# Kernel optimization log

Hardware: AMD Instinct MI355X
Metric: run time of the kernel (lower is better)

## Reference

```python
import jax, jax.numpy as jnp
import numpy as np

B, N, D_IN, D_OUT = 16, 512, 64, 64
TEMP = 1.0
BN_EPS = 1e-5


def setup_inputs() -> dict:
    key = jax.random.key(0)
    ks = jax.random.split(key, 9)
    s_in = 1.0 / np.sqrt(D_IN)
    return {
        "x": jax.random.normal(ks[0], (B, N, D_IN), dtype=jnp.float32),
        # att_proj: Linear(in_dim, out_dim)
        "W_att_proj": jax.random.uniform(ks[1], (D_OUT, D_IN), jnp.float32, -s_in, s_in),
        "b_att_proj": jax.random.uniform(ks[2], (D_OUT,), jnp.float32, -s_in, s_in),
        # att_weight: xavier_normal_ on (out_dim, 1)
        "att_weight": jax.random.normal(ks[3], (D_OUT, 1), jnp.float32) * np.sqrt(2.0 / (D_OUT + 1)),
        "W_with": jax.random.uniform(ks[4], (D_OUT, D_IN), jnp.float32, -s_in, s_in),
        "b_with": jax.random.uniform(ks[5], (D_OUT,), jnp.float32, -s_in, s_in),
        "W_without": jax.random.uniform(ks[6], (D_OUT, D_IN), jnp.float32, -s_in, s_in),
        "b_without": jax.random.uniform(ks[7], (D_OUT,), jnp.float32, -s_in, s_in),
        # BatchNorm1d affine params
        "gamma": jnp.ones((D_OUT,), jnp.float32),
        "beta": jnp.zeros((D_OUT,), jnp.float32),
    }


def reference(x, W_att_proj, b_att_proj, att_weight, W_with, b_with, W_without, b_without, gamma, beta):
    # dropout is identity (eval). Pairwise elementwise product: (B, N_i, N_j, D_in)
    p = x[:, :, None, :] * x[:, None, :, :]
    # score MLP: linear -> tanh -> linear(out_dim -> 1)
    h = jnp.tanh(jnp.einsum("bijd,od->bijo", p, W_att_proj) + b_att_proj)
    s = jnp.einsum("bijo,o->bij", h, att_weight[:, 0]) / TEMP
    # softmax over j (torch dim=-2 of (B,N,N,1))
    a = jax.nn.softmax(s, axis=2)
    # weighted aggregate + projections
    agg = jnp.einsum("bij,bjd->bid", a, x)
    x_out = agg @ W_with.T + b_with + x @ W_without.T + b_without
    # BatchNorm1d over flattened (B*N, D_out), training-mode batch stats
    flat = x_out.reshape(-1, D_OUT)
    mean = jnp.mean(flat, axis=0)
    var = jnp.var(flat, axis=0)
    normed = (flat - mean) * jax.lax.rsqrt(var + BN_EPS) * gamma + beta
    return jax.nn.selu(normed.reshape(B, N, D_OUT))
```

## Files before the change

### kernel.cpp

```cpp
#include <hip/hip_runtime.h>
#include <hip/hip_bf16.h>

#define BB 16
#define NN 512
#define DD 64
#define BN_ROWS (BB * NN)
#define NBIN 32

typedef unsigned short ushort;
typedef unsigned int uint;
typedef short bf16x8 __attribute__((ext_vector_type(8)));
typedef float f32x4  __attribute__((ext_vector_type(4)));

#define K2LOG2E 2.885390081777927f


__device__ __forceinline__ uint pkbf2(float lo, float hi) {
    union { float f; uint u; } a, b; a.f = lo; b.f = hi;
    return __builtin_amdgcn_perm(b.u + 0x8000u, a.u + 0x8000u, 0x07060302u);
}
__device__ __forceinline__ float bflo(uint u) {
    union { uint i; float f; } c; c.i = u << 16; return c.f;
}
__device__ __forceinline__ float bfhi(uint u) {
    union { uint i; float f; } c; c.i = u & 0xffff0000u; return c.f;
}
__device__ __forceinline__ float sigr(float x) {
    return __builtin_amdgcn_rcpf(__builtin_amdgcn_exp2f(x) + 1.0f);
}

__global__ __launch_bounds__(256) void prep_kernel(
    const float* __restrict__ x, const float* __restrict__ Wp,
    float* __restrict__ wpf, ushort* __restrict__ xbf, float* __restrict__ stats)
{
    const int tid = blockIdx.x * 256 + threadIdx.x;
    const int b = tid >> 12, rem = tid & 4095;
    const int jt = rem >> 7, ks = (rem >> 6) & 1, lane = rem & 63;
    const int qd = lane >> 4, ln = lane & 15;
    const float* __restrict__ src =
        x + ((size_t)(b * NN + jt * 16 + ln)) * DD + ks * 32 + qd * 8;
    const float4 v0 = *(const float4*)src;
    const float4 v1 = *(const float4*)(src + 4);
    uint4 o;
    o.x = pkbf2(v0.x, v0.y); o.y = pkbf2(v0.z, v0.w);
    o.z = pkbf2(v1.x, v1.y); o.w = pkbf2(v1.z, v1.w);
    ((uint4*)xbf)[tid] = o;
    if (tid < DD * DD) {
        const int oo = tid >> 6, d = tid & 63;
        const int mt = oo >> 4, l2 = oo & 15;
        const int k2 = d >> 5, q2 = (d >> 3) & 3, e = d & 7;
        wpf[(((mt * 2 + k2) * 64) + (q2 * 16 + l2)) * 8 + e] = Wp[tid] * K2LOG2E;
    }
    if (tid < NBIN * 128) stats[tid] = 0.0f;
}

template <int MINW>
__global__ __launch_bounds__(256, MINW) void attn_kernel(
    const float* __restrict__ x,  const float* __restrict__ wpf,
    const ushort* __restrict__ xbf,
    const float* __restrict__ bp, const float* __restrict__ aw,
    const float* __restrict__ W1, const float* __restrict__ b1,
    const float* __restrict__ W2, const float* __restrict__ b2,
    float* __restrict__ out, float* __restrict__ stats)
{
    __shared__ float part[4][DD];
    __shared__ float s_esum[4];
    __shared__ __align__(16) float s_agg[DD], s_xi[DD];

    const int t = threadIdx.x;
    const int wv = t >> 6, lane = t & 63;
    const int blk = blockIdx.x;
    const int b = (blk & 7) * 2 + ((blk >> 3) & 1);
    const int i = blk >> 4;
    const int row = b * NN + i;
    const int qd = lane >> 4, ln = lane & 15;
    const ushort* __restrict__ xb16 = xbf + (size_t)b * (NN * DD);
    const float* __restrict__ xrow = x + (size_t)row * DD;

    if (t < DD) s_xi[t] = xrow[t];

    float xiv[2][8];
    #pragma unroll
    for (int ks = 0; ks < 2; ++ks) {
        const float4 a = *(const float4*)(xrow + ks * 32 + qd * 8);
        const float4 c = *(const float4*)(xrow + ks * 32 + qd * 8 + 4);
        xiv[ks][0]=a.x; xiv[ks][1]=a.y; xiv[ks][2]=a.z; xiv[ks][3]=a.w;
        xiv[ks][4]=c.x; xiv[ks][5]=c.y; xiv[ks][6]=c.z; xiv[ks][7]=c.w;
    }

    float bpk[16], awk[16];
    #pragma unroll
    for (int mt = 0; mt < 4; ++mt) {
        const float4 vb = *(const float4*)(bp + mt * 16 + qd * 4);
        const float4 va = *(const float4*)(aw + mt * 16 + qd * 4);
        bpk[mt*4+0] = vb.x * K2LOG2E; bpk[mt*4+1] = vb.y * K2LOG2E;
        bpk[mt*4+2] = vb.z * K2LOG2E; bpk[mt*4+3] = vb.w * K2LOG2E;
        awk[mt*4+0] = va.x * -K2LOG2E; awk[mt*4+1] = va.y * -K2LOG2E;
        awk[mt*4+2] = va.z * -K2LOG2E; awk[mt*4+3] = va.w * -K2LOG2E;
    }

    bf16x8 afrag[8];
    #pragma unroll
    for (int g = 0; g < 8; ++g) {
        const int ks = g & 1;
        const float4 wa = *(const float4*)(wpf + (g * 64 + lane) * 8);
        const float4 wb = *(const float4*)(wpf + (g * 64 + lane) * 8 + 4);
        union { bf16x8 v; uint u[4]; } p;
        p.u[0] = pkbf2(wa.x * xiv[ks][0], wa.y * xiv[ks][1]);
        p.u[1] = pkbf2(wa.z * xiv[ks][2], wa.w * xiv[ks][3]);
        p.u[2] = pkbf2(wb.x * xiv[ks][4], wb.y * xiv[ks][5]);
        p.u[3] = pkbf2(wb.z * xiv[ks][6], wb.w * xiv[ks][7]);
        afrag[g] = p.v;
    }

    float vacc[16];
    #pragma unroll
    for (int k = 0; k < 16; ++k) vacc[k] = 0.0f;
    float esum = 0.0f;

    #pragma unroll 4
    for (int tt = 0; tt < 8; ++tt) {
        const int tile = wv * 8 + tt;
        union { bf16x8 v; uint4 u; } b0, b1u;
        b0.v  = *(const bf16x8*)(xb16 + ((tile * 2 + 0) * 64 + lane) * 8);
        b1u.v = *(const bf16x8*)(xb16 + ((tile * 2 + 1) * 64 + lane) * 8);

        float s0 = 0.0f, s1 = 0.0f, s2 = 0.0f, s3 = 0.0f;
        #pragma unroll
        for (int mt = 0; mt < 4; ++mt) {
            f32x4 acc = { bpk[mt*4+0], bpk[mt*4+1], bpk[mt*4+2], bpk[mt*4+3] };
            acc = __builtin_amdgcn_mfma_f32_16x16x32_bf16(afrag[mt*2+0], b0.v,  acc, 0, 0, 0);
            acc = __builtin_amdgcn_mfma_f32_16x16x32_bf16(afrag[mt*2+1], b1u.v, acc, 0, 0, 0);
            s0 = fmaf(awk[mt*4+0], sigr(acc[0]), s0);
            s1 = fmaf(awk[mt*4+1], sigr(acc[1]), s1);
            s2 = fmaf(awk[mt*4+2], sigr(acc[2]), s2);
            s3 = fmaf(awk[mt*4+3], sigr(acc[3]), s3);
        }
        float sj = (s0 + s1) + (s2 + s3);
        sj += __shfl_xor(sj, 16);
        sj += __shfl_xor(sj, 32);

        const float e = __builtin_amdgcn_exp2f(sj);
        esum += e;
        vacc[0]  = fmaf(e, bflo(b0.u.x),  vacc[0]);
        vacc[1]  = fmaf(e, bfhi(b0.u.x),  vacc[1]);
        vacc[2]  = fmaf(e, bflo(b0.u.y),  vacc[2]);
        vacc[3]  = fmaf(e, bfhi(b0.u.y),  vacc[3]);
        vacc[4]  = fmaf(e, bflo(b0.u.z),  vacc[4]);
        vacc[5]  = fmaf(e, bfhi(b0.u.z),  vacc[5]);
        vacc[6]  = fmaf(e, bflo(b0.u.w),  vacc[6]);
        vacc[7]  = fmaf(e, bfhi(b0.u.w),  vacc[7]);
        vacc[8]  = fmaf(e, bflo(b1u.u.x), vacc[8]);
        vacc[9]  = fmaf(e, bfhi(b1u.u.x), vacc[9]);
        vacc[10] = fmaf(e, bflo(b1u.u.y), vacc[10]);
        vacc[11] = fmaf(e, bfhi(b1u.u.y), vacc[11]);
        vacc[12] = fmaf(e, bflo(b1u.u.z), vacc[12]);
        vacc[13] = fmaf(e, bfhi(b1u.u.z), vacc[13]);
        vacc[14] = fmaf(e, bflo(b1u.u.w), vacc[14]);
        vacc[15] = fmaf(e, bfhi(b1u.u.w), vacc[15]);
    }

    #pragma unroll
    for (int off = 1; off < 16; off <<= 1) {
        esum += __shfl_xor(esum, off);
        #pragma unroll
        for (int k = 0; k < 16; ++k)
            vacc[k] += __shfl_xor(vacc[k], off);
    }
    if (lane == 0) s_esum[wv] = esum;
    if (ln == 0) {
        #pragma unroll
        for (int k = 0; k < 16; ++k)
            part[wv][(k >> 3) * 32 + qd * 8 + (k & 7)] = vacc[k];
    }
    __syncthreads();

    if (t < DD) {
        const float tot = (s_esum[0] + s_esum[1]) + (s_esum[2] + s_esum[3]);
        const float inv = 1.0f / tot;
        const float a = (part[0][t] + part[1][t]) + (part[2][t] + part[3][t]);
        s_agg[t] = a * inv;
    }
    __syncthreads();

    {
        const int o = t >> 2, qq = t & 3, d0 = qq * 16;
        const float* __restrict__ w1r = W1 + o * DD + d0;
        const float* __restrict__ w2r = W2 + o * DD + d0;
        float v = 0.0f;
        #pragma unroll
        for (int h = 0; h < 2; ++h) {
            const int dd = h * 8;
            const float4 wa  = *(const float4*)(w1r + dd);
            const float4 wa2 = *(const float4*)(w1r + dd + 4);
            const float4 ag  = *(const float4*)(s_agg + d0 + dd);
            const float4 ag2 = *(const float4*)(s_agg + d0 + dd + 4);
            v = fmaf(wa.x,  ag.x,  v); v = fmaf(wa.y,  ag.y,  v);
            v = fmaf(wa.z,  ag.z,  v); v = fmaf(wa.w,  ag.w,  v);
            v = fmaf(wa2.x, ag2.x, v); v = fmaf(wa2.y, ag2.y, v);
            v = fmaf(wa2.z, ag2.z, v); v = fmaf(wa2.w, ag2.w, v);
            const float4 wb  = *(const float4*)(w2r + dd);
            const float4 wb2 = *(const float4*)(w2r + dd + 4);
            const float4 xi  = *(const float4*)(s_xi + d0 + dd);
            const float4 xi2 = *(const float4*)(s_xi + d0 + dd + 4);
            v = fmaf(wb.x,  xi.x,  v); v = fmaf(wb.y,  xi.y,  v);
            v = fmaf(wb.z,  xi.z,  v); v = fmaf(wb.w,  xi.w,  v);
            v = fmaf(wb2.x, xi2.x, v); v = fmaf(wb2.y, xi2.y, v);
            v = fmaf(wb2.z, xi2.z, v); v = fmaf(wb2.w, xi2.w, v);
        }
        v += __shfl_xor(v, 1);
        v += __shfl_xor(v, 2);
        if (qq == 0) {
            v += b1[o] + b2[o];
            out[(size_t)row * DD + o] = v;
            float* __restrict__ sb = stats + (blk & (NBIN - 1)) * 128;
            atomicAdd(&sb[o], v);
            atomicAdd(&sb[64 + o], v * v);
        }
    }
}

__global__ __launch_bounds__(256) void final_kernel(
    const float* __restrict__ stats,
    const float* __restrict__ gamma, const float* __restrict__ beta,
    float* __restrict__ out)
{
    __shared__ float smu[DD], sga[DD], sbe[DD];
    if (threadIdx.x < DD) {
        const int o = threadIdx.x;
        float s1 = 0.0f, s2 = 0.0f;
        #pragma unroll 8
        for (int bin = 0; bin < NBIN; ++bin) {
            s1 += stats[bin * 128 + o];
            s2 += stats[bin * 128 + 64 + o];
        }
        const float mean = s1 * (1.0f / BN_ROWS);
        const float var  = s2 * (1.0f / BN_ROWS) - mean * mean;
        smu[o] = mean;
        sga[o] = gamma[o] / sqrtf(var + 1e-5f);
        sbe[o] = beta[o];
    }
    __syncthreads();
    const int i4 = blockIdx.x * 256 + threadIdx.x;
    const int o0 = (i4 & 15) * 4;
    const float4 v = ((const float4*)out)[i4];
    float r[4] = { v.x, v.y, v.z, v.w };
    #pragma unroll
    for (int c = 0; c < 4; ++c) {
        const float nrm = (r[c] - smu[o0 + c]) * sga[o0 + c] + sbe[o0 + c];
        r[c] = nrm > 0.0f
            ? 1.0507009873554805f * nrm
            : 1.7580993408473766f * expm1f(nrm);
    }
    ((float4*)out)[i4] = make_float4(r[0], r[1], r[2], r[3]);
}

extern "C" void kernel_launch(void* const* d_in, const int* in_sizes, int n_in,
                              void* d_out, int out_size, void* d_ws, size_t ws_size,
                              hipStream_t stream)
{
    const float* x  = (const float*)d_in[0];
    const float* Wp = (const float*)d_in[1];
    const float* bp = (const float*)d_in[2];
    const float* aw = (const float*)d_in[3];
    const float* W1 = (const float*)d_in[4];
    const float* b1 = (const float*)d_in[5];
    const float* W2 = (const float*)d_in[6];
    const float* b2 = (const float*)d_in[7];
    const float* ga = (const float*)d_in[8];
    const float* be = (const float*)d_in[9];

    float*  stats = (float*)d_ws;
    float*  wpf   = stats + NBIN * 128;
    ushort* xbf   = (ushort*)(wpf + DD * DD);
    float*  out   = (float*)d_out;

    typedef void (*attn_fn)(const float*, const float*, const ushort*,
                            const float*, const float*,
                            const float*, const float*,
                            const float*, const float*,
                            float*, float*);
    static attn_fn chosen = nullptr;
    if (!chosen) {
        attn_fn cands[4] = { attn_kernel<7>, attn_kernel<6>,
                             attn_kernel<5>, attn_kernel<3> };
        chosen = cands[3];
        for (int c = 0; c < 4; ++c) {
            hipFuncAttributes fa;
            if (hipFuncGetAttributes(&fa,
                    reinterpret_cast<const void*>(cands[c])) == hipSuccess
                && fa.localSizeBytes == 0) {
                chosen = cands[c];
                break;
            }
        }
    }

    prep_kernel<<<256, 256, 0, stream>>>(x, Wp, wpf, xbf, stats);
    chosen<<<BN_ROWS, 256, 0, stream>>>(x, wpf, xbf, bp, aw, W1, b1, W2, b2, out, stats);
    final_kernel<<<512, 256, 0, stream>>>(stats, ga, be, out);
}
```

Baseline: 183.2 us.

## Widen prep kernel, add MFMA priority hints, parallelize BN stat reduction

The prep kernel now launches twice as many threads, and each one converts a single float4 to bf16 instead of two. The attention inner loop wraps its MFMA and sigmoid section in s_setprio(1)/s_setprio(0) so that wave gets issue priority. The final kernel now splits the reduction of the 32 stat bins across all 256 threads, using a two-group shared-memory partial sum instead of a serial loop in 64 threads. These target small overheads in the prep and final kernels and scheduling in the main loop, at the cost of an extra __syncthreads.

```diff
diff --git a/kernel.cpp b/kernel.cpp
--- a/kernel.cpp
+++ b/kernel.cpp
@@ -34,17 +34,16 @@
     float* __restrict__ wpf, ushort* __restrict__ xbf, float* __restrict__ stats)
 {
     const int tid = blockIdx.x * 256 + threadIdx.x;
-    const int b = tid >> 12, rem = tid & 4095;
+    const int tid16 = tid >> 1, sub = tid & 1;
+    const int b = tid16 >> 12, rem = tid16 & 4095;
     const int jt = rem >> 7, ks = (rem >> 6) & 1, lane = rem & 63;
     const int qd = lane >> 4, ln = lane & 15;
     const float* __restrict__ src =
-        x + ((size_t)(b * NN + jt * 16 + ln)) * DD + ks * 32 + qd * 8;
-    const float4 v0 = *(const float4*)src;
-    const float4 v1 = *(const float4*)(src + 4);
-    uint4 o;
-    o.x = pkbf2(v0.x, v0.y); o.y = pkbf2(v0.z, v0.w);
-    o.z = pkbf2(v1.x, v1.y); o.w = pkbf2(v1.z, v1.w);
-    ((uint4*)xbf)[tid] = o;
+        x + ((size_t)(b * NN + jt * 16 + ln)) * DD + ks * 32 + qd * 8 + sub * 4;
+    const float4 v = *(const float4*)src;
+    uint2 o;
+    o.x = pkbf2(v.x, v.y); o.y = pkbf2(v.z, v.w);
+    ((uint2*)xbf)[tid] = o;
     if (tid < DD * DD) {
         const int oo = tid >> 6, d = tid & 63;
         const int mt = oo >> 4, l2 = oo & 15;
@@ -126,6 +125,7 @@
         b1u.v = *(const bf16x8*)(xb16 + ((tile * 2 + 1) * 64 + lane) * 8);
 
         float s0 = 0.0f, s1 = 0.0f, s2 = 0.0f, s3 = 0.0f;
+        __builtin_amdgcn_s_setprio(1);
         #pragma unroll
         for (int mt = 0; mt < 4; ++mt) {
             f32x4 acc = { bpk[mt*4+0], bpk[mt*4+1], bpk[mt*4+2], bpk[mt*4+3] };
@@ -136,6 +136,7 @@
             s2 = fmaf(awk[mt*4+2], sigr(acc[2]), s2);
             s3 = fmaf(awk[mt*4+3], sigr(acc[3]), s3);
         }
+        __builtin_amdgcn_s_setprio(0);
         float sj = (s0 + s1) + (s2 + s3);
         sj += __shfl_xor(sj, 16);
         sj += __shfl_xor(sj, 32);
@@ -225,15 +226,21 @@
     const float* __restrict__ gamma, const float* __restrict__ beta,
     float* __restrict__ out)
 {
+    __shared__ float red[2][128];
     __shared__ float smu[DD], sga[DD], sbe[DD];
+    {
+        const int slot = threadIdx.x & 127, grp = threadIdx.x >> 7;
+        float s = 0.0f;
+        #pragma unroll
+        for (int bb = 0; bb < NBIN / 2; ++bb)
+            s += stats[(grp * (NBIN / 2) + bb) * 128 + slot];
+        red[grp][slot] = s;
+    }
+    __syncthreads();
     if (threadIdx.x < DD) {
         const int o = threadIdx.x;
-        float s1 = 0.0f, s2 = 0.0f;
-        #pragma unroll 8
-        for (int bin = 0; bin < NBIN; ++bin) {
-            s1 += stats[bin * 128 + o];
-            s2 += stats[bin * 128 + 64 + o];
-        }
+        const float s1 = red[0][o] + red[1][o];
+        const float s2 = red[0][64 + o] + red[1][64 + o];
         const float mean = s1 * (1.0f / BN_ROWS);
         const float var  = s2 * (1.0f / BN_ROWS) - mean * mean;
         smu[o] = mean;
@@ -296,7 +303,7 @@
         }
     }
 
-    prep_kernel<<<256, 256, 0, stream>>>(x, Wp, wpf, xbf, stats);
+    prep_kernel<<<512, 256, 0, stream>>>(x, Wp, wpf, xbf, stats);
     chosen<<<BN_ROWS, 256, 0, stream>>>(x, wpf, xbf, bp, aw, W1, b1, W2, b2, out, stats);
     final_kernel<<<512, 256, 0, stream>>>(stats, ga, be, out);
 }
```

Measured after the change: 190.8 us. 1.04x slower.
